# Kernel tuning notes

Measured on AMD Instinct MI355X. Metric: run time of the kernel, lower is better.

## Reference

```python
import jax, jax.numpy as jnp
import numpy as np

N, E, F0, H = 100000, 3200000, 256, 128
TEMP = 2.0
ALPHA = 0.2  # leaky relu slope
EPS_BN = 1e-5
EPS_LN = 1e-5


def spmm(vals, row, col, X):
    # sparse [N,N] @ dense [N,D] via gather + segment_sum
    return jax.ops.segment_sum(vals[:, None] * X[col], row, num_segments=N)


def batchnorm(h, g, b):
    mu = jnp.mean(h, axis=0, keepdims=True)
    var = jnp.var(h, axis=0, keepdims=True)
    return (h - mu) * jax.lax.rsqrt(var + EPS_BN) * g + b


def layernorm(h, g, b):
    mu = jnp.mean(h, axis=-1, keepdims=True)
    var = jnp.var(h, axis=-1, keepdims=True)
    return (h - mu) * jax.lax.rsqrt(var + EPS_LN) * g + b


def setup_inputs() -> dict:
    key = jax.random.key(0)
    ks = jax.random.split(key, 32)
    x = jax.random.normal(ks[0], (N, F0), dtype=jnp.float32)
    edge_row = jax.random.randint(ks[1], (E,), 0, N)
    edge_col = jax.random.randint(ks[2], (E,), 0, N)
    adj_vals = jax.random.uniform(ks[3], (E,), dtype=jnp.float32) / 32.0  # ~normalized adj
    sf = lambda k, sh: jax.random.normal(k, sh, dtype=jnp.float32) * 0.05
    in_dim = 3 * F0 + 1
    return {
        "x": x, "edge_row": edge_row, "edge_col": edge_col, "adj_vals": adj_vals,
        # LowPassExtractor (GCN)
        "W_gc1": sf(ks[4], (F0, 2 * H)), "b_gc1": jnp.zeros((2 * H,), jnp.float32),
        "bn1_g": jnp.ones((2 * H,), jnp.float32), "bn1_b": jnp.zeros((2 * H,), jnp.float32),
        "W_gc2": sf(ks[5], (2 * H, H)), "b_gc2": jnp.zeros((H,), jnp.float32),
        "bn2_g": jnp.ones((H,), jnp.float32), "bn2_b": jnp.zeros((H,), jnp.float32),
        # Gating
        "Wg1": sf(ks[6], (in_dim, H)), "bg1": jnp.zeros((H,), jnp.float32),
        "ln_g": jnp.ones((H,), jnp.float32), "ln_b": jnp.zeros((H,), jnp.float32),
        "Wg2": sf(ks[7], (H, 2)), "bg2": jnp.zeros((2,), jnp.float32),
        # HighPassExpert
        "Wxp": sf(ks[8], (F0, H)), "bxp": jnp.zeros((H,), jnp.float32),
        "res_scale": jnp.asarray(1.0, jnp.float32),
        "rn_g": jnp.ones((H,), jnp.float32), "rn_b": jnp.zeros((H,), jnp.float32),
        "Wq": sf(ks[9], (H, H)), "Wk": sf(ks[10], (H, H)), "Wv": sf(ks[11], (H, H)),
    }


def reference(x, edge_row, edge_col, adj_vals,
              W_gc1, b_gc1, bn1_g, bn1_b, W_gc2, b_gc2, bn2_g, bn2_b,
              Wg1, bg1, ln_g, ln_b, Wg2, bg2,
              Wxp, bxp, res_scale, rn_g, rn_b, Wq, Wk, Wv):
    # ---- LowPassExtractor: two GCN layers (spmm(adj, xW)+b) with batchnorm+relu
    h1 = jax.nn.relu(batchnorm(spmm(adj_vals, edge_row, edge_col, x @ W_gc1) + b_gc1, bn1_g, bn1_b))
    low = jax.nn.relu(batchnorm(spmm(adj_vals, edge_row, edge_col, h1 @ W_gc2) + b_gc2, bn2_g, bn2_b))

    # ---- Gating: neighborhood stats via spmm
    AX = spmm(adj_vals, edge_row, edge_col, x)
    deg = jax.ops.segment_sum(adj_vals, edge_row, num_segments=N)[:, None]
    x_mean = AX / (deg + 1e-8)
    AX2 = spmm(adj_vals, edge_row, edge_col, x * x)
    var = AX2 / (deg + 1e-8) - x_mean * x_mean
    x_std = jnp.sqrt(jnp.clip(var, 0.0))
    x_cat = jnp.concatenate([x, AX - x, x_std, deg], axis=1)  # [N, 3*F0+1]
    hg = jax.nn.relu(layernorm(x_cat @ Wg1 + bg1, ln_g, ln_b))
    gate = jax.nn.softmax((hg @ Wg2 + bg2) / TEMP, axis=1)  # [N, 2]

    # ---- HighPassExpert: GAT-style sparse attention on normalized residual
    residual = layernorm(res_scale * (x @ Wxp + bxp - low), rn_g, rn_b)
    Q, K, V = residual @ Wq, residual @ Wk, residual @ Wv
    scores = jnp.sum(Q[edge_row] * K[edge_col], axis=1) / jnp.sqrt(jnp.float32(H))
    exp_s = jnp.exp(jnp.where(scores > 0, scores, ALPHA * scores))
    denom = jax.ops.segment_sum(exp_s, edge_row, num_segments=N)
    attn = exp_s / (denom[edge_row] + 1e-16)
    high = jax.ops.segment_sum(attn[:, None] * V[edge_col], edge_row, num_segments=N)

    output = gate[:, 0:1] * low + gate[:, 1:2] * high
    return output, gate, low, high
```

## Files before the change

### kernel.cpp

```cpp
#include <hip/hip_runtime.h>

#define F0 256
#define HD 128
#define NP 100352

typedef unsigned short u16;
typedef __attribute__((ext_vector_type(8))) short short8;
typedef __attribute__((ext_vector_type(4))) float f32x4;

__device__ inline float bf2f(u16 u) {
    union { unsigned int i; float f; } v; v.i = ((unsigned int)u) << 16; return v.f;
}
__device__ inline u16 f2bf(float f) {
    union { float f; unsigned int i; } v; v.f = f;
    unsigned int r = v.i + 0x7FFF + ((v.i >> 16) & 1);
    return (u16)(r >> 16);
}

__device__ inline float rsum16(float v) {
    v += __shfl_xor(v, 1); v += __shfl_xor(v, 2);
    v += __shfl_xor(v, 4); v += __shfl_xor(v, 8);
    return v;
}

#define GLOAD16(gp, lp) __builtin_amdgcn_global_load_lds( \
    (const __attribute__((address_space(1))) void*)(gp), \
    (__attribute__((address_space(3))) void*)(lp), 16, 0, 0)

__global__ void k_hist_rank(const int* __restrict__ row, int* __restrict__ counts,
                            int* __restrict__ rank, int E) {
    int e = blockIdx.x * blockDim.x + threadIdx.x;
    if (e < E) rank[e] = atomicAdd(&counts[row[e]], 1);
}

__global__ void k_scan_blk(const int* __restrict__ counts, int* __restrict__ scan_out,
                           int* __restrict__ partials, int n) {
    __shared__ int wsum[16];
    int t = threadIdx.x;
    int i = blockIdx.x * 1024 + t;
    int v = (i < n) ? counts[i] : 0;
    int lane = t & 63, w = t >> 6;
    #pragma unroll
    for (int off = 1; off < 64; off <<= 1) { int u = __shfl_up(v, off); if (lane >= off) v += u; }
    if (lane == 63) wsum[w] = v;
    __syncthreads();
    if (t < 16) {
        int s = wsum[t];
        #pragma unroll
        for (int off = 1; off < 16; off <<= 1) { int u = __shfl_up(s, off); if (t >= off) s += u; }
        wsum[t] = s;
    }
    __syncthreads();
    int add = (w > 0) ? wsum[w - 1] : 0;
    if (i < n) scan_out[i] = v + add;
    if (t == 1023) partials[blockIdx.x] = wsum[15];
}

__global__ void k_scan_part(int* partials, int nb) {
    __shared__ int ws2[2];
    int t = threadIdx.x;
    int v = (t < nb) ? partials[t] : 0;
    int lane = t & 63, w = t >> 6;
    #pragma unroll
    for (int off = 1; off < 64; off <<= 1) { int u = __shfl_up(v, off); if (lane >= off) v += u; }
    if (lane == 63) ws2[w] = v;
    __syncthreads();
    if (w == 1) v += ws2[0];
    if (t < nb) partials[t] = v;
}

__global__ void k_scan_add(int* __restrict__ row_ptr, const int* __restrict__ partials, int n) {
    int b = blockIdx.x;
    int i = b * 1024 + threadIdx.x;
    if (b == 0 && threadIdx.x == 0) row_ptr[0] = 0;
    int add = (b > 0) ? partials[b - 1] : 0;
    if (i < n) row_ptr[1 + i] += add;
}

__global__ void k_scatter_direct(const int* __restrict__ row, const int* __restrict__ ecol,
                                 const float* __restrict__ avals, const int* __restrict__ rank,
                                 const int* __restrict__ row_ptr, int2* __restrict__ cv, int E) {
    int e = blockIdx.x * blockDim.x + threadIdx.x;
    if (e >= E) return;
    int r = row[e];
    int pos = row_ptr[r] + rank[e];
    cv[pos] = make_int2(ecol[e], __float_as_int(avals[e]));
}

__global__ void k_cast_x(const float* __restrict__ x, u16* __restrict__ xb, int total4) {
    int i = blockIdx.x * blockDim.x + threadIdx.x;
    if (i >= total4) return;
    float4 v = ((const float4*)x)[i];
    ((ushort4*)xb)[i] = make_ushort4(f2bf(v.x), f2bf(v.y), f2bf(v.z), f2bf(v.w));
}

__global__ void k_prep_w(const float* __restrict__ W_gc1, const float* __restrict__ W_gc2,
                         const float* __restrict__ Wg1, const float* __restrict__ Wxp,
                         const float* __restrict__ Wq, const float* __restrict__ Wk,
                         const float* __restrict__ Wv,
                         u16* Wgc1t, u16* Wgc2t, u16* Wdt, u16* W1t, u16* W2t,
                         u16* Wxpt, u16* Wqt, u16* Wkt, u16* Wvt) {
    int z = blockIdx.z;
    int idx = blockIdx.x * 256 + threadIdx.x;
    if (z == 0) { if (idx < 65536) { int n = idx >> 8, k = idx & 255; Wgc1t[idx] = f2bf(W_gc1[k * 256 + n]); } }
    else if (z == 1) { if (idx < 32768) { int n = idx >> 8, k = idx & 255; Wgc2t[idx] = f2bf(W_gc2[k * 128 + n]); } }
    else if (z == 2) { if (idx < 32768) { int n = idx >> 8, k = idx & 255; Wdt[idx] = f2bf(Wg1[k * 128 + n] - Wg1[(k + 256) * 128 + n]); } }
    else if (z == 3) { if (idx < 32768) { int n = idx >> 8, k = idx & 255; W1t[idx] = f2bf(Wg1[(k + 256) * 128 + n]); } }
    else if (z == 4) { if (idx < 32768) { int n = idx >> 8, k = idx & 255; W2t[idx] = f2bf(Wg1[(k + 512) * 128 + n]); } }
    else if (z == 5) { if (idx < 32768) { int n = idx >> 8, k = idx & 255; Wxpt[idx] = f2bf(Wxp[k * 128 + n]); } }
    else if (z == 6) { if (idx < 16384) { int n = idx >> 7, k = idx & 127; Wqt[idx] = f2bf(Wq[k * 128 + n]); } }
    else if (z == 7) { if (idx < 16384) { int n = idx >> 7, k = idx & 127; Wkt[idx] = f2bf(Wk[k * 128 + n]); } }
    else if (z == 8) { if (idx < 16384) { int n = idx >> 7, k = idx & 127; Wvt[idx] = f2bf(Wv[k * 128 + n]); } }
}

__global__ void k_spmm_x2(const u16* __restrict__ Xb, const int* __restrict__ row_ptr,
                          const int2* __restrict__ cv,
                          u16* __restrict__ AXb, u16* __restrict__ XSTDb,
                          float* __restrict__ deg, int N) {
    int wid = blockIdx.x * 4 + (threadIdx.x >> 6);
    if (wid >= N) return;
    int lane = threadIdx.x & 63;
    float a0 = 0, a1 = 0, a2 = 0, a3 = 0;
    float q0 = 0, q1 = 0, q2 = 0, q3 = 0, d = 0;
    int s = row_ptr[wid], e = row_ptr[wid + 1];
    int j = s;
    for (; j + 7 < e; j += 8) {
        int2 cc[8]; ushort4 xb[8];
        #pragma unroll
        for (int t = 0; t < 8; ++t) cc[t] = cv[j + t];
        #pragma unroll
        for (int t = 0; t < 8; ++t) xb[t] = *(const ushort4*)(Xb + (size_t)cc[t].x * F0 + lane * 4);
        #pragma unroll
        for (int t = 0; t < 8; ++t) {
            float x0 = bf2f(xb[t].x), x1 = bf2f(xb[t].y), x2 = bf2f(xb[t].z), x3 = bf2f(xb[t].w);
            float vv = __int_as_float(cc[t].y);
            a0 += vv * x0; a1 += vv * x1; a2 += vv * x2; a3 += vv * x3;
            q0 += vv * x0 * x0; q1 += vv * x1 * x1; q2 += vv * x2 * x2; q3 += vv * x3 * x3;
            d += vv;
        }
    }
    for (; j + 3 < e; j += 4) {
        int2 cc[4]; ushort4 xb[4];
        #pragma unroll
        for (int t = 0; t < 4; ++t) cc[t] = cv[j + t];
        #pragma unroll
        for (int t = 0; t < 4; ++t) xb[t] = *(const ushort4*)(Xb + (size_t)cc[t].x * F0 + lane * 4);
        #pragma unroll
        for (int t = 0; t < 4; ++t) {
            float x0 = bf2f(xb[t].x), x1 = bf2f(xb[t].y), x2 = bf2f(xb[t].z), x3 = bf2f(xb[t].w);
            float vv = __int_as_float(cc[t].y);
            a0 += vv * x0; a1 += vv * x1; a2 += vv * x2; a3 += vv * x3;
            q0 += vv * x0 * x0; q1 += vv * x1 * x1; q2 += vv * x2 * x2; q3 += vv * x3 * x3;
            d += vv;
        }
    }
    for (; j < e; ++j) {
        int2 cc = cv[j];
        float v0 = __int_as_float(cc.y);
        ushort4 xb0 = *(const ushort4*)(Xb + (size_t)cc.x * F0 + lane * 4);
        float x0 = bf2f(xb0.x), x1 = bf2f(xb0.y), x2 = bf2f(xb0.z), x3 = bf2f(xb0.w);
        a0 += v0 * x0; a1 += v0 * x1; a2 += v0 * x2; a3 += v0 * x3;
        q0 += v0 * x0 * x0; q1 += v0 * x1 * x1; q2 += v0 * x2 * x2; q3 += v0 * x3 * x3;
        d += v0;
    }
    float inv = 1.0f / (d + 1e-8f);
    float m0 = a0 * inv, m1 = a1 * inv, m2 = a2 * inv, m3 = a3 * inv;
    float s0 = sqrtf(fmaxf(q0 * inv - m0 * m0, 0.f));
    float s1 = sqrtf(fmaxf(q1 * inv - m1 * m1, 0.f));
    float s2 = sqrtf(fmaxf(q2 * inv - m2 * m2, 0.f));
    float s3 = sqrtf(fmaxf(q3 * inv - m3 * m3, 0.f));
    *(ushort4*)(AXb + (size_t)wid * F0 + lane * 4) = make_ushort4(f2bf(a0), f2bf(a1), f2bf(a2), f2bf(a3));
    *(ushort4*)(XSTDb + (size_t)wid * F0 + lane * 4) = make_ushort4(f2bf(s0), f2bf(s1), f2bf(s2), f2bf(s3));
    if (lane == 0) deg[wid] = d;
}

__global__ void k_spmm128(const u16* __restrict__ Xb, const int* __restrict__ row_ptr,
                          const int2* __restrict__ cv, u16* __restrict__ OUT, int N) {
    int wid = blockIdx.x * 4 + (threadIdx.x >> 6);
    if (wid >= N) return;
    int lane = threadIdx.x & 63;
    float a0 = 0, a1 = 0;
    int s = row_ptr[wid], e = row_ptr[wid + 1];
    int j = s;
    for (; j + 7 < e; j += 8) {
        int2 cc[8]; ushort2 xb[8];
        #pragma unroll
        for (int t = 0; t < 8; ++t) cc[t] = cv[j + t];
        #pragma unroll
        for (int t = 0; t < 8; ++t) xb[t] = *(const ushort2*)(Xb + (size_t)cc[t].x * HD + lane * 2);
        #pragma unroll
        for (int t = 0; t < 8; ++t) {
            float vv = __int_as_float(cc[t].y);
            a0 += vv * bf2f(xb[t].x); a1 += vv * bf2f(xb[t].y);
        }
    }
    for (; j + 3 < e; j += 4) {
        int2 cc[4]; ushort2 xb[4];
        #pragma unroll
        for (int t = 0; t < 4; ++t) cc[t] = cv[j + t];
        #pragma unroll
        for (int t = 0; t < 4; ++t) xb[t] = *(const ushort2*)(Xb + (size_t)cc[t].x * HD + lane * 2);
        #pragma unroll
        for (int t = 0; t < 4; ++t) {
            float vv = __int_as_float(cc[t].y);
            a0 += vv * bf2f(xb[t].x); a1 += vv * bf2f(xb[t].y);
        }
    }
    for (; j < e; ++j) {
        int2 cc = cv[j];
        float v0 = __int_as_float(cc.y);
        ushort2 x0 = *(const ushort2*)(Xb + (size_t)cc.x * HD + lane * 2);
        a0 += v0 * bf2f(x0.x); a1 += v0 * bf2f(x0.y);
    }
    *(ushort2*)(OUT + (size_t)wid * HD + lane * 2) = make_ushort2(f2bf(a0), f2bf(a1));
}

__device__ inline void mm_core(const u16* __restrict__ A, const u16* __restrict__ Bt,
                               int K, int ldA, int ldB, int m0, int n0,
                               u16* As, u16* Bs, f32x4 acc[4][4]) {
    int t = threadIdx.x, w = t >> 6, l = t & 63;
    int wr = (w >> 1) * 64, wc = (w & 1) * 64;
    int aoff = (wr + (l & 15)) * 32 + (l >> 4) * 8;
    int boff = (wc + (l & 15)) * 32 + (l >> 4) * 8;
    for (int k0 = 0; k0 < K; k0 += 32) {
        __syncthreads();
        #pragma unroll
        for (int s = 0; s < 2; ++s) {
            int i = s * 256 + t;
            int row = i >> 2, ch = i & 3;
            GLOAD16(A + (size_t)(m0 + row) * ldA + k0 + ch * 8, As + i * 8);
            GLOAD16(Bt + (size_t)(n0 + row) * ldB + k0 + ch * 8, Bs + i * 8);
        }
        __syncthreads();
        short8 af[4], bfr[4];
        #pragma unroll
        for (int i = 0; i < 4; ++i) af[i] = *(const short8*)(As + aoff + i * 16 * 32);
        #pragma unroll
        for (int j = 0; j < 4; ++j) bfr[j] = *(const short8*)(Bs + boff + j * 16 * 32);
        #pragma unroll
        for (int i = 0; i < 4; ++i)
            #pragma unroll
            for (int j = 0; j < 4; ++j)
                acc[i][j] = __builtin_amdgcn_mfma_f32_16x16x32_bf16(af[i], bfr[j], acc[i][j], 0, 0, 0);
    }
}

__device__ inline void mm_zero(f32x4 acc[4][4]) {
    #pragma unroll
    for (int i = 0; i < 4; ++i)
        #pragma unroll
        for (int j = 0; j < 4; ++j)
            acc[i][j] = (f32x4){0.f, 0.f, 0.f, 0.f};
}

__global__ __launch_bounds__(256) void k_mm_bf(const u16* __restrict__ A, const u16* __restrict__ Bt,
                                               u16* __restrict__ C, int M, int K, int Nc) {
    __shared__ __align__(16) u16 As[128 * 32];
    __shared__ __align__(16) u16 Bs[128 * 32];
    int m0 = blockIdx.x * 128, n0 = blockIdx.y * 128;
    f32x4 acc[4][4]; mm_zero(acc);
    mm_core(A, Bt, K, K, K, m0, n0, As, Bs, acc);
    int t = threadIdx.x, w = t >> 6, l = t & 63;
    int rbase = m0 + (w >> 1) * 64 + (l >> 4) * 4;
    int cbase = n0 + (w & 1) * 64 + (l & 15);
    #pragma unroll
    for (int j = 0; j < 4; ++j)
        #pragma unroll
        for (int i = 0; i < 4; ++i)
            #pragma unroll
            for (int r = 0; r < 4; ++r) {
                int row = rbase + i * 16 + r;
                if (row < M) C[(size_t)row * Nc + cbase + j * 16] = f2bf(acc[i][j][r]);
            }
}

__global__ __launch_bounds__(256) void k_mm_gate(const u16* A0, const u16* A1, const u16* A2,
                                                 const u16* B0, const u16* B1, const u16* B2,
                                                 const float* __restrict__ bg1,
                                                 const float* __restrict__ wlast,
                                                 const float* __restrict__ deg,
                                                 const float* __restrict__ ln_g,
                                                 const float* __restrict__ ln_b,
                                                 const float* __restrict__ Wg2,
                                                 const float* __restrict__ bg2,
                                                 float* __restrict__ gate, int M) {
    __shared__ __align__(16) u16 As[128 * 32];
    __shared__ __align__(16) u16 Bs[128 * 32];
    __shared__ float ps1[2][128], ps2[2][128], pt0[2][128], pt1[2][128];
    int m0 = blockIdx.x * 128;
    f32x4 acc[4][4]; mm_zero(acc);
    mm_core(A0, B0, 256, 256, 256, m0, 0, As, Bs, acc);
    mm_core(A1, B1, 256, 256, 256, m0, 0, As, Bs, acc);
    mm_core(A2, B2, 256, 256, 256, m0, 0, As, Bs, acc);
    int t = threadIdx.x, w = t >> 6, l = t & 63;
    int hcol = w & 1;
    int lr0 = (w >> 1) * 64 + (l >> 4) * 4;
    int cbase = hcol * 64 + (l & 15);
    float wl[4], bg[4], lg[4], lb[4], wa[4], wb_[4];
    #pragma unroll
    for (int j = 0; j < 4; ++j) {
        int col = cbase + j * 16;
        wl[j] = wlast[col]; bg[j] = bg1[col];
        lg[j] = ln_g[col];  lb[j] = ln_b[col];
        wa[j] = Wg2[col * 2 + 0]; wb_[j] = Wg2[col * 2 + 1];
    }
    #pragma unroll
    for (int i = 0; i < 4; ++i)
        #pragma unroll
        for (int r = 0; r < 4; ++r) {
            int row = m0 + lr0 + i * 16 + r;
            float dgv = (row < M) ? deg[row] : 0.f;
            float s1 = 0.f, s2 = 0.f;
            #pragma unroll
            for (int j = 0; j < 4; ++j) {
                float h = acc[i][j][r] + bg[j] + dgv * wl[j];
                acc[i][j][r] = h;
                s1 += h; s2 += h * h;
            }
            s1 = rsum16(s1); s2 = rsum16(s2);
            if ((l & 15) == 0) { ps1[hcol][lr0 + i * 16 + r] = s1; ps2[hcol][lr0 + i * 16 + r] = s2; }
        }
    __syncthreads();
    #pragma unroll
    for (int i = 0; i < 4; ++i)
        #pragma unroll
        for (int r = 0; r < 4; ++r) {
            int lr = lr0 + i * 16 + r;
            float s1 = ps1[0][lr] + ps1[1][lr];
            float s2 = ps2[0][lr] + ps2[1][lr];
            float mu = s1 * (1.f / 128.f);
            float var = s2 * (1.f / 128.f) - mu * mu;
            float is = 1.0f / sqrtf(var + 1e-5f);
            float t0 = 0.f, t1 = 0.f;
            #pragma unroll
            for (int j = 0; j < 4; ++j) {
                float y = fmaxf((acc[i][j][r] - mu) * is * lg[j] + lb[j], 0.f);
                t0 += y * wa[j]; t1 += y * wb_[j];
            }
            t0 = rsum16(t0); t1 = rsum16(t1);
            if ((l & 15) == 0) { pt0[hcol][lr] = t0; pt1[hcol][lr] = t1; }
        }
    __syncthreads();
    if (hcol == 0 && (l & 15) == 0) {
        float b20 = bg2[0], b21 = bg2[1];
        #pragma unroll
        for (int i = 0; i < 4; ++i)
            #pragma unroll
            for (int r = 0; r < 4; ++r) {
                int lr = lr0 + i * 16 + r;
                int row = m0 + lr;
                if (row >= M) continue;
                float t0 = (pt0[0][lr] + pt0[1][lr] + b20) * 0.5f;
                float t1 = (pt1[0][lr] + pt1[1][lr] + b21) * 0.5f;
                float m = fmaxf(t0, t1);
                float e0 = __expf(t0 - m), e1 = __expf(t1 - m);
                float inv = 1.0f / (e0 + e1);
                gate[(size_t)row * 2 + 0] = e0 * inv;
                gate[(size_t)row * 2 + 1] = e1 * inv;
            }
    }
}

__global__ __launch_bounds__(256) void k_mm_xp(const u16* __restrict__ A, const u16* __restrict__ Bt,
                                               const float* __restrict__ bias,
                                               const float* __restrict__ low,
                                               const float* __restrict__ g,
                                               const float* __restrict__ b,
                                               const float* __restrict__ rs_ptr,
                                               u16* __restrict__ resid, int M) {
    __shared__ __align__(16) u16 As[128 * 32];
    __shared__ __align__(16) u16 Bs[128 * 32];
    __shared__ float ps1[2][128], ps2[2][128];
    int m0 = blockIdx.x * 128;
    f32x4 acc[4][4]; mm_zero(acc);
    mm_core(A, Bt, 256, 256, 256, m0, 0, As, Bs, acc);
    int t = threadIdx.x, w = t >> 6, l = t & 63;
    int hcol = w & 1;
    int lr0 = (w >> 1) * 64 + (l >> 4) * 4;
    int cbase = hcol * 64 + (l & 15);
    float rs = rs_ptr[0];
    float bx[4], lg[4], lb[4];
    #pragma unroll
    for (int j = 0; j < 4; ++j) {
        int col = cbase + j * 16;
        bx[j] = bias[col]; lg[j] = g[col]; lb[j] = b[col];
    }
    #pragma unroll
    for (int i = 0; i < 4; ++i)
        #pragma unroll
        for (int r = 0; r < 4; ++r) {
            int row = m0 + lr0 + i * 16 + r;
            float s1 = 0.f, s2 = 0.f;
            #pragma unroll
            for (int j = 0; j < 4; ++j) {
                float lv = (row < M) ? low[(size_t)row * 128 + cbase + j * 16] : 0.f;
                float h = rs * (acc[i][j][r] + bx[j] - lv);
                acc[i][j][r] = h;
                s1 += h; s2 += h * h;
            }
            s1 = rsum16(s1); s2 = rsum16(s2);
            if ((l & 15) == 0) { ps1[hcol][lr0 + i * 16 + r] = s1; ps2[hcol][lr0 + i * 16 + r] = s2; }
        }
    __syncthreads();
    #pragma unroll
    for (int i = 0; i < 4; ++i)
        #pragma unroll
        for (int r = 0; r < 4; ++r) {
            int lr = lr0 + i * 16 + r;
            int row = m0 + lr;
            float s1 = ps1[0][lr] + ps1[1][lr];
            float s2 = ps2[0][lr] + ps2[1][lr];
            float mu = s1 * (1.f / 128.f);
            float var = s2 * (1.f / 128.f) - mu * mu;
            float is = 1.0f / sqrtf(var + 1e-5f);
            if (row < M) {
                #pragma unroll
                for (int j = 0; j < 4; ++j) {
                    float y = (acc[i][j][r] - mu) * is * lg[j] + lb[j];
                    resid[(size_t)row * 128 + cbase + j * 16] = f2bf(y);
                }
            }
        }
}

__global__ __launch_bounds__(256) void k_mm_qkv(const u16* __restrict__ A,
                                                const u16* Wqt, const u16* Wkt, const u16* Wvt,
                                                u16* Qb, u16* KV, int M) {
    __shared__ __align__(16) u16 As[128 * 32];
    __shared__ __align__(16) u16 Bs[128 * 32];
    int z = blockIdx.z;
    const u16* Bt = (z == 0) ? Wqt : (z == 1) ? Wkt : Wvt;
    int m0 = blockIdx.x * 128;
    f32x4 acc[4][4]; mm_zero(acc);
    mm_core(A, Bt, 128, 128, 128, m0, 0, As, Bs, acc);
    int t = threadIdx.x, w = t >> 6, l = t & 63;
    int rbase = m0 + (w >> 1) * 64 + (l >> 4) * 4;
    int cbase = (w & 1) * 64 + (l & 15);
    if (z == 0) {
        #pragma unroll
        for (int j = 0; j < 4; ++j)
            #pragma unroll
            for (int i = 0; i < 4; ++i)
                #pragma unroll
                for (int r = 0; r < 4; ++r) {
                    int row = rbase + i * 16 + r;
                    if (row < M) Qb[(size_t)row * 128 + cbase + j * 16] = f2bf(acc[i][j][r]);
                }
    } else {
        int coff = (z == 1) ? 0 : 128;
        #pragma unroll
        for (int j = 0; j < 4; ++j)
            #pragma unroll
            for (int i = 0; i < 4; ++i)
                #pragma unroll
                for (int r = 0; r < 4; ++r) {
                    int row = rbase + i * 16 + r;
                    if (row < M) KV[(size_t)row * 256 + coff + cbase + j * 16] = f2bf(acc[i][j][r]);
                }
    }
}

__global__ void k_bn_stats_bf(const u16* __restrict__ H, double* __restrict__ stats, int N, int C) {
    int t = threadIdx.x;
    int rpt = 256 / C;
    int rsub = t / C;
    int col = t - rsub * C;
    double s = 0.0, q = 0.0;
    for (long r = (long)blockIdx.x * rpt + rsub; r < N; r += (long)gridDim.x * rpt) {
        float v = bf2f(H[(size_t)r * C + col]);
        s += v; q += (double)v * v;
    }
    __shared__ double sh_s[256], sh_q[256];
    sh_s[t] = s; sh_q[t] = q;
    __syncthreads();
    if (t < C) {
        for (int k = 1; k < rpt; ++k) { s += sh_s[t + k * C]; q += sh_q[t + k * C]; }
        atomicAdd(&stats[t], s);
        atomicAdd(&stats[C + t], q);
    }
}

__global__ void k_bn_fin(const double* __restrict__ stats, const float* __restrict__ g,
                         const float* __restrict__ b, float* __restrict__ scale,
                         float* __restrict__ shift, int C, double invN) {
    int t = threadIdx.x;
    if (t >= C) return;
    double mean = stats[t] * invN;
    double var = stats[C + t] * invN - mean * mean;
    float sc = (float)((double)g[t] / sqrt(var + 1e-5));
    scale[t] = sc;
    shift[t] = b[t] - (float)mean * sc;
}

__global__ void k_bn_relu_bb(const u16* __restrict__ in, u16* __restrict__ out,
                             const float* __restrict__ scale, const float* __restrict__ shift,
                             int total4, int cmask4) {
    int i = blockIdx.x * blockDim.x + threadIdx.x;
    if (i >= total4) return;
    int c4 = i & cmask4;
    ushort4 v = ((const ushort4*)in)[i];
    float4 sc = ((const float4*)scale)[c4];
    float4 sh = ((const float4*)shift)[c4];
    ((ushort4*)out)[i] = make_ushort4(
        f2bf(fmaxf(bf2f(v.x) * sc.x + sh.x, 0.f)), f2bf(fmaxf(bf2f(v.y) * sc.y + sh.y, 0.f)),
        f2bf(fmaxf(bf2f(v.z) * sc.z + sh.z, 0.f)), f2bf(fmaxf(bf2f(v.w) * sc.w + sh.w, 0.f)));
}

__global__ void k_bn_relu_bf(const u16* __restrict__ in, float* __restrict__ out,
                             const float* __restrict__ scale, const float* __restrict__ shift,
                             int total4, int cmask4) {
    int i = blockIdx.x * blockDim.x + threadIdx.x;
    if (i >= total4) return;
    int c4 = i & cmask4;
    ushort4 v = ((const ushort4*)in)[i];
    float4 sc = ((const float4*)scale)[c4];
    float4 sh = ((const float4*)shift)[c4];
    ((float4*)out)[i] = make_float4(
        fmaxf(bf2f(v.x) * sc.x + sh.x, 0.f), fmaxf(bf2f(v.y) * sc.y + sh.y, 0.f),
        fmaxf(bf2f(v.z) * sc.z + sh.z, 0.f), fmaxf(bf2f(v.w) * sc.w + sh.w, 0.f));
}

__global__ void k_attn_aggr(const u16* __restrict__ Qb, const u16* __restrict__ KV,
                            const int* __restrict__ row_ptr, const int2* __restrict__ cv,
                            const float* __restrict__ gate, const float* __restrict__ low,
                            float* __restrict__ high, float* __restrict__ outp, int N) {
    int wid = blockIdx.x * 4 + (threadIdx.x >> 6);
    if (wid >= N) return;
    int lane = threadIdx.x & 63;
    int sub = lane & 15;
    int g = lane >> 4;
    float qs[8];
    {
        short8 q8 = *(const short8*)(Qb + (size_t)wid * HD + sub * 8);
        #pragma unroll
        for (int k = 0; k < 8; ++k) qs[k] = bf2f((u16)q8[k]);
    }
    float2 qv;
    {
        ushort2 qt = *(const ushort2*)(Qb + (size_t)wid * HD + lane * 2);
        qv.x = bf2f(qt.x); qv.y = bf2f(qt.y);
    }
    float n0 = 0, n1 = 0, den = 0;
    int s = row_ptr[wid], e = row_ptr[wid + 1];
    int j = s;
    for (; j + 7 < e; j += 8) {
        int cg0 = cv[j + g].x;
        int cg1 = cv[j + 4 + g].x;
        short8 ka = *(const short8*)(KV + (size_t)cg0 * 256 + sub * 8);
        short8 kb = *(const short8*)(KV + (size_t)cg1 * 256 + sub * 8);
        float p0 = qs[0] * bf2f((u16)ka[0]) + qs[1] * bf2f((u16)ka[1])
                 + qs[2] * bf2f((u16)ka[2]) + qs[3] * bf2f((u16)ka[3])
                 + qs[4] * bf2f((u16)ka[4]) + qs[5] * bf2f((u16)ka[5])
                 + qs[6] * bf2f((u16)ka[6]) + qs[7] * bf2f((u16)ka[7]);
        float p1 = qs[0] * bf2f((u16)kb[0]) + qs[1] * bf2f((u16)kb[1])
                 + qs[2] * bf2f((u16)kb[2]) + qs[3] * bf2f((u16)kb[3])
                 + qs[4] * bf2f((u16)kb[4]) + qs[5] * bf2f((u16)kb[5])
                 + qs[6] * bf2f((u16)kb[6]) + qs[7] * bf2f((u16)kb[7]);
        p0 += __shfl_xor(p0, 1); p1 += __shfl_xor(p1, 1);
        p0 += __shfl_xor(p0, 2); p1 += __shfl_xor(p1, 2);
        p0 += __shfl_xor(p0, 4); p1 += __shfl_xor(p1, 4);
        p0 += __shfl_xor(p0, 8); p1 += __shfl_xor(p1, 8);
        float sc0 = p0 * 0.08838834764831845f;
        float sc1 = p1 * 0.08838834764831845f;
        float ls0 = sc0 > 0.f ? sc0 : 0.2f * sc0;
        float ls1 = sc1 > 0.f ? sc1 : 0.2f * sc1;
        float ex0 = __expf(ls0);
        float ex1 = __expf(ls1);
        float exb[8]; int cb[8];
        #pragma unroll
        for (int t = 0; t < 4; ++t) {
            exb[t]     = __shfl(ex0, t << 4); cb[t]     = __shfl(cg0, t << 4);
            exb[4 + t] = __shfl(ex1, t << 4); cb[4 + t] = __shfl(cg1, t << 4);
        }
        ushort2 vb[8];
        #pragma unroll
        for (int t = 0; t < 8; ++t) vb[t] = *(const ushort2*)(KV + (size_t)cb[t] * 256 + 128 + lane * 2);
        #pragma unroll
        for (int t = 0; t < 8; ++t) {
            n0 += exb[t] * bf2f(vb[t].x);
            n1 += exb[t] * bf2f(vb[t].y);
            den += exb[t];
        }
    }
    for (; j + 3 < e; j += 4) {
        int cg = cv[j + g].x;
        short8 kk = *(const short8*)(KV + (size_t)cg * 256 + sub * 8);
        float p = qs[0] * bf2f((u16)kk[0]) + qs[1] * bf2f((u16)kk[1])
                + qs[2] * bf2f((u16)kk[2]) + qs[3] * bf2f((u16)kk[3])
                + qs[4] * bf2f((u16)kk[4]) + qs[5] * bf2f((u16)kk[5])
                + qs[6] * bf2f((u16)kk[6]) + qs[7] * bf2f((u16)kk[7]);
        p += __shfl_xor(p, 1); p += __shfl_xor(p, 2);
        p += __shfl_xor(p, 4); p += __shfl_xor(p, 8);
        float sc = p * 0.08838834764831845f;
        float ls = sc > 0.f ? sc : 0.2f * sc;
        float ex = __expf(ls);
        float exb[4]; int cb[4];
        #pragma unroll
        for (int t = 0; t < 4; ++t) { exb[t] = __shfl(ex, t << 4); cb[t] = __shfl(cg, t << 4); }
        ushort2 vb[4];
        #pragma unroll
        for (int t = 0; t < 4; ++t) vb[t] = *(const ushort2*)(KV + (size_t)cb[t] * 256 + 128 + lane * 2);
        #pragma unroll
        for (int t = 0; t < 4; ++t) {
            n0 += exb[t] * bf2f(vb[t].x);
            n1 += exb[t] * bf2f(vb[t].y);
            den += exb[t];
        }
    }
    for (; j < e; ++j) {
        int c0 = cv[j].x;
        ushort2 kb0 = *(const ushort2*)(KV + (size_t)c0 * 256 + lane * 2);
        ushort2 vb0 = *(const ushort2*)(KV + (size_t)c0 * 256 + 128 + lane * 2);
        float sc0 = qv.x * bf2f(kb0.x) + qv.y * bf2f(kb0.y);
        #pragma unroll
        for (int off = 32; off > 0; off >>= 1) sc0 += __shfl_xor(sc0, off);
        float p = sc0 * 0.08838834764831845f;
        float ls = p > 0.f ? p : 0.2f * p;
        float ex = __expf(ls);
        n0 += ex * bf2f(vb0.x); n1 += ex * bf2f(vb0.y); den += ex;
    }
    float inv = 1.0f / (den + 1e-16f);
    float h0 = n0 * inv, h1 = n1 * inv;
    *(float2*)(high + (size_t)wid * HD + lane * 2) = make_float2(h0, h1);
    float g0 = gate[(size_t)wid * 2 + 0], g1 = gate[(size_t)wid * 2 + 1];
    float2 lw = *(const float2*)(low + (size_t)wid * HD + lane * 2);
    *(float2*)(outp + (size_t)wid * HD + lane * 2) = make_float2(g0 * lw.x + g1 * h0, g0 * lw.y + g1 * h1);
}

extern "C" void kernel_launch(void* const* d_in, const int* in_sizes, int n_in,
                              void* d_out, int out_size, void* d_ws, size_t ws_size,
                              hipStream_t stream) {
    const float* x      = (const float*)d_in[0];
    const int*   erow   = (const int*)d_in[1];
    const int*   ecol   = (const int*)d_in[2];
    const float* avals  = (const float*)d_in[3];
    const float* W_gc1  = (const float*)d_in[4];
    const float* bn1_g  = (const float*)d_in[6];
    const float* bn1_b  = (const float*)d_in[7];
    const float* W_gc2  = (const float*)d_in[8];
    const float* bn2_g  = (const float*)d_in[10];
    const float* bn2_b  = (const float*)d_in[11];
    const float* Wg1    = (const float*)d_in[12];
    const float* bg1    = (const float*)d_in[13];
    const float* ln_g   = (const float*)d_in[14];
    const float* ln_b   = (const float*)d_in[15];
    const float* Wg2    = (const float*)d_in[16];
    const float* bg2    = (const float*)d_in[17];
    const float* Wxp    = (const float*)d_in[18];
    const float* bxp    = (const float*)d_in[19];
    const float* rscale = (const float*)d_in[20];
    const float* rn_g   = (const float*)d_in[21];
    const float* rn_b   = (const float*)d_in[22];
    const float* Wq     = (const float*)d_in[23];
    const float* Wk     = (const float*)d_in[24];
    const float* Wv     = (const float*)d_in[25];

    const int N = in_sizes[0] / F0;
    const int E = in_sizes[1];

    char* base = (char*)d_ws;
    size_t off = 0;
    auto carve = [&](size_t bytes) -> char* {
        char* p = base + off;
        off += (bytes + 255) & ~(size_t)255;
        return p;
    };
    double* stats  = (double*)carve(4096);
    float* scaleb  = (float*)carve(1024);
    float* shiftb  = (float*)carve(1024);
    int*   partials= (int*)carve(2048);
    u16* Wgc1t = (u16*)carve(65536 * 2);
    u16* Wgc2t = (u16*)carve(32768 * 2);
    u16* Wdt   = (u16*)carve(32768 * 2);
    u16* W1t   = (u16*)carve(32768 * 2);
    u16* W2t   = (u16*)carve(32768 * 2);
    u16* Wxpt  = (u16*)carve(32768 * 2);
    u16* Wqt   = (u16*)carve(16384 * 2);
    u16* Wkt   = (u16*)carve(16384 * 2);
    u16* Wvt   = (u16*)carve(16384 * 2);
    int*   row_ptr = (int*)carve((size_t)(N + 1) * 4);
    int*   cursor  = (int*)carve((size_t)N * 4);
    float* deg     = (float*)carve((size_t)N * 4);
    int2*  cv      = (int2*)carve((size_t)E * 8);
    u16*   x_bf    = (u16*)carve((size_t)NP * F0 * 2);
    u16*   kvb     = (u16*)carve((size_t)NP * 256 * 2);
    u16*   AX_bf   = (u16*)carve((size_t)NP * F0 * 2);
    u16*   XSTD_bf = (u16*)carve((size_t)NP * F0 * 2);
    u16*   h1_bf   = (u16*)carve((size_t)NP * F0 * 2);
    u16*   S2_bf   = (u16*)carve((size_t)NP * HD * 2);
    u16*   G2_bf   = (u16*)carve((size_t)NP * HD * 2);
    float* M3      = (float*)carve((size_t)NP * HD * 4);
    (void)ws_size; (void)n_in; (void)out_size;

    u16*   S1_bf = h1_bf;
    u16*   resid_bf = h1_bf;
    int*   rank  = (int*)M3;
    u16*   Qb    = (u16*)M3;

    float* out_o    = (float*)d_out;
    float* out_gate = out_o + (size_t)N * HD;
    float* out_low  = out_gate + (size_t)N * 2;
    float* out_high = out_low + (size_t)N * HD;

    const int eb  = (E + 255) / 256;
    const int wb  = (N + 3) / 4;
    const int NB1 = (N + 1023) / 1024;
    const int gx  = (N + 127) / 128;
    const dim3 blk(256);

    hipMemsetAsync(cursor, 0, (size_t)N * 4, stream);
    k_hist_rank<<<eb, blk, 0, stream>>>(erow, cursor, rank, E);
    k_scan_blk<<<NB1, 1024, 0, stream>>>(cursor, row_ptr + 1, partials, N);
    k_scan_part<<<1, 128, 0, stream>>>(partials, NB1);
    k_scan_add<<<NB1, 1024, 0, stream>>>(row_ptr, partials, N);
    k_scatter_direct<<<eb, blk, 0, stream>>>(erow, ecol, avals, rank, row_ptr, cv, E);

    k_cast_x<<<(N * 64 + 255) / 256, blk, 0, stream>>>(x, x_bf, N * 64);
    k_prep_w<<<dim3(256, 1, 9), blk, 0, stream>>>(W_gc1, W_gc2, Wg1, Wxp, Wq, Wk, Wv,
                                                  Wgc1t, Wgc2t, Wdt, W1t, W2t, Wxpt, Wqt, Wkt, Wvt);

    k_spmm_x2<<<wb, blk, 0, stream>>>(x_bf, row_ptr, cv, AX_bf, XSTD_bf, deg, N);

    k_mm_bf<<<dim3(gx, 2), blk, 0, stream>>>(AX_bf, Wgc1t, S1_bf, N, 256, 256);
    hipMemsetAsync(stats, 0, 4096, stream);
    k_bn_stats_bf<<<1024, blk, 0, stream>>>(S1_bf, stats, N, 256);
    k_bn_fin<<<1, blk, 0, stream>>>(stats, bn1_g, bn1_b, scaleb, shiftb, 256, 1.0 / N);
    k_bn_relu_bb<<<(N * 64 + 255) / 256, blk, 0, stream>>>(S1_bf, h1_bf, scaleb, shiftb, N * 64, 63);
    k_mm_bf<<<dim3(gx, 1), blk, 0, stream>>>(h1_bf, Wgc2t, G2_bf, N, 256, 128);
    k_spmm128<<<wb, blk, 0, stream>>>(G2_bf, row_ptr, cv, S2_bf, N);
    hipMemsetAsync(stats, 0, 2048, stream);
    k_bn_stats_bf<<<1024, blk, 0, stream>>>(S2_bf, stats, N, 128);
    k_bn_fin<<<1, blk, 0, stream>>>(stats, bn2_g, bn2_b, scaleb, shiftb, 128, 1.0 / N);
    k_bn_relu_bf<<<(N * 32 + 255) / 256, blk, 0, stream>>>(S2_bf, out_low, scaleb, shiftb, N * 32, 31);

    k_mm_gate<<<dim3(gx, 1), blk, 0, stream>>>(x_bf, AX_bf, XSTD_bf, Wdt, W1t, W2t,
                                               bg1, Wg1 + (size_t)768 * 128, deg,
                                               ln_g, ln_b, Wg2, bg2, out_gate, N);

    k_mm_xp<<<dim3(gx, 1), blk, 0, stream>>>(x_bf, Wxpt, bxp, out_low, rn_g, rn_b, rscale,
                                             resid_bf, N);
    k_mm_qkv<<<dim3(gx, 1, 3), blk, 0, stream>>>(resid_bf, Wqt, Wkt, Wvt, Qb, kvb, N);
    k_attn_aggr<<<wb, blk, 0, stream>>>(Qb, kvb, row_ptr, cv, out_gate, out_low, out_high, out_o, N);
}
```

Before: 1.410 ms.

## Fuse QKV projections into one kernel reusing the A tile; trim SpMM tails

Replaces the three-way z-grid QKV matmul with a single kernel that loads each 128-row block of the residual into shared memory once and reuses it for Q, K and V. This cuts redundant reads of the activation matrix, at the cost of more shared memory per block and a serial loop over the three weights. The CSR scatter now uses nontemporal loads for its streamed edge arrays. The 4-wide unrolled remainder loops in both SpMM kernels are removed, so leftovers after the 8-wide loop fall to the scalar loop.

```diff
diff --git a/kernel.cpp b/kernel.cpp
--- a/kernel.cpp
+++ b/kernel.cpp
@@ -83,8 +83,11 @@
     int e = blockIdx.x * blockDim.x + threadIdx.x;
     if (e >= E) return;
     int r = row[e];
-    int pos = row_ptr[r] + rank[e];
-    cv[pos] = make_int2(ecol[e], __float_as_int(avals[e]));
+    int c = __builtin_nontemporal_load(ecol + e);
+    float v = __builtin_nontemporal_load(avals + e);
+    int rk = __builtin_nontemporal_load(rank + e);
+    int pos = row_ptr[r] + rk;
+    cv[pos] = make_int2(c, __float_as_int(v));
 }
 
 __global__ void k_cast_x(const float* __restrict__ x, u16* __restrict__ xb, int total4) {
@@ -139,21 +142,6 @@
             d += vv;
         }
     }
-    for (; j + 3 < e; j += 4) {
-        int2 cc[4]; ushort4 xb[4];
-        #pragma unroll
-        for (int t = 0; t < 4; ++t) cc[t] = cv[j + t];
-        #pragma unroll
-        for (int t = 0; t < 4; ++t) xb[t] = *(const ushort4*)(Xb + (size_t)cc[t].x * F0 + lane * 4);
-        #pragma unroll
-        for (int t = 0; t < 4; ++t) {
-            float x0 = bf2f(xb[t].x), x1 = bf2f(xb[t].y), x2 = bf2f(xb[t].z), x3 = bf2f(xb[t].w);
-            float vv = __int_as_float(cc[t].y);
-            a0 += vv * x0; a1 += vv * x1; a2 += vv * x2; a3 += vv * x3;
-            q0 += vv * x0 * x0; q1 += vv * x1 * x1; q2 += vv * x2 * x2; q3 += vv * x3 * x3;
-            d += vv;
-        }
-    }
     for (; j < e; ++j) {
         int2 cc = cv[j];
         float v0 = __int_as_float(cc.y);
@@ -190,18 +178,6 @@
         for (int t = 0; t < 8; ++t) xb[t] = *(const ushort2*)(Xb + (size_t)cc[t].x * HD + lane * 2);
         #pragma unroll
         for (int t = 0; t < 8; ++t) {
-            float vv = __int_as_float(cc[t].y);
-            a0 += vv * bf2f(xb[t].x); a1 += vv * bf2f(xb[t].y);
-        }
-    }
-    for (; j + 3 < e; j += 4) {
-        int2 cc[4]; ushort2 xb[4];
-        #pragma unroll
-        for (int t = 0; t < 4; ++t) cc[t] = cv[j + t];
-        #pragma unroll
-        for (int t = 0; t < 4; ++t) xb[t] = *(const ushort2*)(Xb + (size_t)cc[t].x * HD + lane * 2);
-        #pragma unroll
-        for (int t = 0; t < 4; ++t) {
             float vv = __int_as_float(cc[t].y);
             a0 += vv * bf2f(xb[t].x); a1 += vv * bf2f(xb[t].y);
         }
@@ -423,40 +399,75 @@
         }
 }
 
-__global__ __launch_bounds__(256) void k_mm_qkv(const u16* __restrict__ A,
-                                                const u16* Wqt, const u16* Wkt, const u16* Wvt,
-                                                u16* Qb, u16* KV, int M) {
-    __shared__ __align__(16) u16 As[128 * 32];
+__global__ __launch_bounds__(256) void k_mm_qkv3(const u16* __restrict__ A,
+                                                 const u16* __restrict__ Wqt,
+                                                 const u16* __restrict__ Wkt,
+                                                 const u16* __restrict__ Wvt,
+                                                 u16* __restrict__ Qb, u16* __restrict__ KV, int M) {
+    __shared__ __align__(16) u16 As[4][128 * 32];
     __shared__ __align__(16) u16 Bs[128 * 32];
-    int z = blockIdx.z;
-    const u16* Bt = (z == 0) ? Wqt : (z == 1) ? Wkt : Wvt;
     int m0 = blockIdx.x * 128;
-    f32x4 acc[4][4]; mm_zero(acc);
-    mm_core(A, Bt, 128, 128, 128, m0, 0, As, Bs, acc);
     int t = threadIdx.x, w = t >> 6, l = t & 63;
+    #pragma unroll
+    for (int c = 0; c < 4; ++c)
+        #pragma unroll
+        for (int s = 0; s < 2; ++s) {
+            int i = s * 256 + t;
+            int row = i >> 2, ch = i & 3;
+            GLOAD16(A + (size_t)(m0 + row) * 128 + c * 32 + ch * 8, As[c] + i * 8);
+        }
+    int wr = (w >> 1) * 64, wc = (w & 1) * 64;
+    int aoff = (wr + (l & 15)) * 32 + (l >> 4) * 8;
+    int boff = (wc + (l & 15)) * 32 + (l >> 4) * 8;
     int rbase = m0 + (w >> 1) * 64 + (l >> 4) * 4;
     int cbase = (w & 1) * 64 + (l & 15);
-    if (z == 0) {
-        #pragma unroll
-        for (int j = 0; j < 4; ++j)
+    #pragma unroll
+    for (int z = 0; z < 3; ++z) {
+        const u16* Bt = (z == 0) ? Wqt : (z == 1) ? Wkt : Wvt;
+        f32x4 acc[4][4]; mm_zero(acc);
+        for (int k0 = 0; k0 < 128; k0 += 32) {
+            __syncthreads();
+            #pragma unroll
+            for (int s = 0; s < 2; ++s) {
+                int i = s * 256 + t;
+                int row = i >> 2, ch = i & 3;
+                GLOAD16(Bt + (size_t)row * 128 + k0 + ch * 8, Bs + i * 8);
+            }
+            __syncthreads();
+            const u16* Ac = As[k0 >> 5];
+            short8 af[4], bfr[4];
+            #pragma unroll
+            for (int i = 0; i < 4; ++i) af[i] = *(const short8*)(Ac + aoff + i * 16 * 32);
+            #pragma unroll
+            for (int j = 0; j < 4; ++j) bfr[j] = *(const short8*)(Bs + boff + j * 16 * 32);
             #pragma unroll
             for (int i = 0; i < 4; ++i)
                 #pragma unroll
-                for (int r = 0; r < 4; ++r) {
-                    int row = rbase + i * 16 + r;
-                    if (row < M) Qb[(size_t)row * 128 + cbase + j * 16] = f2bf(acc[i][j][r]);
-                }
-    } else {
-        int coff = (z == 1) ? 0 : 128;
-        #pragma unroll
-        for (int j = 0; j < 4; ++j)
-            #pragma unroll
-            for (int i = 0; i < 4; ++i)
+                for (int j = 0; j < 4; ++j)
+                    acc[i][j] = __builtin_amdgcn_mfma_f32_16x16x32_bf16(af[i], bfr[j], acc[i][j], 0, 0, 0);
+        }
+        if (z == 0) {
+            #pragma unroll
+            for (int j = 0; j < 4; ++j)
                 #pragma unroll
-                for (int r = 0; r < 4; ++r) {
-                    int row = rbase + i * 16 + r;
-                    if (row < M) KV[(size_t)row * 256 + coff + cbase + j * 16] = f2bf(acc[i][j][r]);
-                }
+                for (int i = 0; i < 4; ++i)
+                    #pragma unroll
+                    for (int r = 0; r < 4; ++r) {
+                        int row = rbase + i * 16 + r;
+                        if (row < M) Qb[(size_t)row * 128 + cbase + j * 16] = f2bf(acc[i][j][r]);
+                    }
+        } else {
+            int coff = (z == 1) ? 0 : 128;
+            #pragma unroll
+            for (int j = 0; j < 4; ++j)
+                #pragma unroll
+                for (int i = 0; i < 4; ++i)
+                    #pragma unroll
+                    for (int r = 0; r < 4; ++r) {
+                        int row = rbase + i * 16 + r;
+                        if (row < M) KV[(size_t)row * 256 + coff + cbase + j * 16] = f2bf(acc[i][j][r]);
+                    }
+        }
     }
 }
 
@@ -739,6 +750,6 @@
 
     k_mm_xp<<<dim3(gx, 1), blk, 0, stream>>>(x_bf, Wxpt, bxp, out_low, rn_g, rn_b, rscale,
                                              resid_bf, N);
-    k_mm_qkv<<<dim3(gx, 1, 3), blk, 0, stream>>>(resid_bf, Wqt, Wkt, Wvt, Qb, kvb, N);
+    k_mm_qkv3<<<dim3(gx, 1), blk, 0, stream>>>(resid_bf, Wqt, Wkt, Wvt, Qb, kvb, N);
     k_attn_aggr<<<wb, blk, 0, stream>>>(Qb, kvb, row_ptr, cv, out_gate, out_low, out_high, out_o, N);
 }
```

After: 1.530 ms. +8.5%, slower.
